# Kernel tuning notes

Hardware: AMD Instinct MI355X
Metric: run time of the kernel (lower is better)

The kernel has to match this reference:

```python
import jax, jax.numpy as jnp
import numpy as np

N = 50000   # nodes
E = 600000  # edges
D = 128     # in_channels
H = 32      # MLP hidden


def setup_inputs() -> dict:
    key = jax.random.key(0)
    ks = jax.random.split(key, 10)
    x = jax.random.normal(ks[0], (N, D), dtype=jnp.float32)
    edge_index = jax.random.randint(ks[1], (2, E), 0, N, dtype=jnp.int32)
    W_gcn = jax.random.normal(ks[2], (D, D), dtype=jnp.float32) / np.sqrt(D)
    b_gcn = jnp.zeros((D,), dtype=jnp.float32)
    w1 = jax.random.normal(ks[3], (D, H), dtype=jnp.float32) / np.sqrt(D)
    b1 = jnp.zeros((H,), dtype=jnp.float32)
    w2 = jax.random.normal(ks[4], (H, H), dtype=jnp.float32) / np.sqrt(H)
    b2 = jnp.zeros((H,), dtype=jnp.float32)
    w3 = jax.random.normal(ks[5], (H, 1), dtype=jnp.float32) / np.sqrt(H)
    b3 = jnp.zeros((1,), dtype=jnp.float32)
    return {"x": x, "edge_index": edge_index, "W_gcn": W_gcn, "b_gcn": b_gcn,
            "w1": w1, "b1": b1, "w2": w2, "b2": b2, "w3": w3, "b3": b3}


def _gcn_conv(x, edge_index, W, b):
    """PyG GCNConv: add self-loops, symmetric D^-1/2 (A+I) D^-1/2 normalization."""
    xw = x @ W  # [N, D]
    loop = jnp.arange(N, dtype=edge_index.dtype)
    row = jnp.concatenate([edge_index[0], loop])  # source
    col = jnp.concatenate([edge_index[1], loop])  # target
    deg = jax.ops.segment_sum(jnp.ones_like(col, dtype=xw.dtype), col, num_segments=N)
    dinv = jnp.where(deg > 0, jax.lax.rsqrt(deg), 0.0)
    norm = dinv[row] * dinv[col]              # [E+N]
    msg = xw[row] * norm[:, None]             # gather + scale, [E+N, D]
    out = jax.ops.segment_sum(msg, col, num_segments=N)  # scatter-add, [N, D]
    return out + b


def reference(x, edge_index, W_gcn, b_gcn, w1, b1, w2, b2, w3, b3):
    out = jax.nn.relu(_gcn_conv(x, edge_index, W_gcn, b_gcn))
    h = out + x                               # residual
    h = jax.nn.relu(h @ w1 + b1)
    h = jax.nn.relu(h @ w2 + b2)
    return h @ w3 + b3                        # [N, 1]
```

## Files before the change

kernel.cpp:

```cpp
#include <hip/hip_runtime.h>

#define DIM 128
#define HID 32
#define CAP 64
#define NFILL 512

typedef __attribute__((ext_vector_type(8))) short v8s;
typedef __attribute__((ext_vector_type(8))) unsigned short v8u;
typedef __attribute__((ext_vector_type(4))) float v4f;
typedef __attribute__((ext_vector_type(4))) int v4i;

static __device__ __forceinline__ unsigned short f2bf(float f) {
    unsigned int u = __float_as_uint(f);
    u += 0x7fffu + ((u >> 16) & 1u);
    return (unsigned short)(u >> 16);
}

__global__ __launch_bounds__(256) void prep_kernel(int2* __restrict__ csn,
                                                   const float* __restrict__ W,
                                                   unsigned short* __restrict__ wbt,
                                                   int n) {
    int gtid = (int)blockIdx.x * 256 + threadIdx.x;
    int nthr = (int)gridDim.x * 256;
    for (int i = gtid * 2; i < n; i += nthr * 2) {
        if (i + 1 < n) {
            *(int4*)&csn[i] = make_int4(0, 0, 0, 0);
        } else {
            csn[i] = make_int2(0, 0);
        }
    }
    for (int f = gtid; f < DIM * DIM; f += nthr) {
        int k = f >> 7, nn = f & 127;
        wbt[nn * 128 + k] = f2bf(W[f]);
    }
}

__global__ __launch_bounds__(256, 8) void gemm_fill_kernel(const float* __restrict__ x,
                                                           const unsigned short* __restrict__ wbt,
                                                           signed char* __restrict__ xwq,
                                                           int2* __restrict__ csn,
                                                           const int* __restrict__ ei,
                                                           int* __restrict__ srcs,
                                                           int n, int E) {
    int t = threadIdx.x;
    int b = (int)blockIdx.x;
    if (b < NFILL) {
        const int* col = ei + E;
        int* cnt = (int*)csn;
        const int xcd = b & 7;
        const int s = b >> 3;
        const int nslice = NFILL >> 3;
        const int octs = (E + 7) >> 3;
        const int ops = (octs + nslice - 1) / nslice;
        const int o0 = s * ops;
        const int o1 = min(o0 + ops, octs);
        for (int oi = o0 + t; oi < o1; oi += 256) {
            int base = oi * 8;
            if (base + 7 < E) {
                v4i ra = __builtin_nontemporal_load((const v4i*)&ei[base]);
                v4i rb = __builtin_nontemporal_load((const v4i*)&ei[base + 4]);
                v4i ca = __builtin_nontemporal_load((const v4i*)&col[base]);
                v4i cb = __builtin_nontemporal_load((const v4i*)&col[base + 4]);
#pragma unroll
                for (int u = 0; u < 4; ++u) {
                    int cc = ca[u];
                    if ((cc & 7) == xcd) {
                        int p = atomicAdd(&cnt[cc * 2], 1);
                        if (p < CAP) srcs[(cc << 6) + p] = ra[u];
                    }
                }
#pragma unroll
                for (int u = 0; u < 4; ++u) {
                    int cc = cb[u];
                    if ((cc & 7) == xcd) {
                        int p = atomicAdd(&cnt[cc * 2], 1);
                        if (p < CAP) srcs[(cc << 6) + p] = rb[u];
                    }
                }
            } else {
                for (int e = base; e < E; ++e) {
                    int cc = col[e];
                    if ((cc & 7) == xcd) {
                        int p = atomicAdd(&cnt[cc * 2], 1);
                        if (p < CAP) srcs[(cc << 6) + p] = ei[e];
                    }
                }
            }
        }
    } else {
        int tile = b - NFILL;
        int row0 = tile * 64;
        int w = t >> 6;
        int l = t & 63;
        int q = l >> 4;
        int mn = l & 15;
        int row = row0 + w * 16 + mn;

        v8s afrag[4];
        const float* xr = x + (size_t)row * DIM + q * 8;
#pragma unroll
        for (int kt = 0; kt < 4; ++kt) {
            float4 qa = make_float4(0.f, 0.f, 0.f, 0.f), qb = qa;
            if (row < n) {
                const float4* s4 = (const float4*)(xr + kt * 32);
                qa = s4[0];
                qb = s4[1];
            }
            v8u pk;
            pk[0] = f2bf(qa.x); pk[1] = f2bf(qa.y); pk[2] = f2bf(qa.z); pk[3] = f2bf(qa.w);
            pk[4] = f2bf(qb.x); pk[5] = f2bf(qb.y); pk[6] = f2bf(qb.z); pk[7] = f2bf(qb.w);
            afrag[kt] = (v8s)pk;
        }

        v4f acc[8];
        const unsigned short* wr = wbt + mn * 128 + q * 8;
#pragma unroll
        for (int ct = 0; ct < 8; ++ct) {
            acc[ct] = (v4f){0.f, 0.f, 0.f, 0.f};
#pragma unroll
            for (int kt = 0; kt < 4; ++kt) {
                v8s bfrag = *(const v8s*)(wr + ct * (16 * 128) + kt * 32);
                acc[ct] = __builtin_amdgcn_mfma_f32_16x16x32_bf16(afrag[kt], bfrag, acc[ct], 0, 0, 0);
            }
        }

        float m[4];
#pragma unroll
        for (int i = 0; i < 4; ++i) {
            float mm = 0.f;
#pragma unroll
            for (int ct = 0; ct < 8; ++ct) mm = fmaxf(mm, fabsf(acc[ct][i]));
            m[i] = mm;
        }
#pragma unroll
        for (int off = 1; off < 16; off <<= 1) {
#pragma unroll
            for (int i = 0; i < 4; ++i) m[i] = fmaxf(m[i], __shfl_xor(m[i], off));
        }
        float inv[4];
#pragma unroll
        for (int i = 0; i < 4; ++i) {
            m[i] = fmaxf(m[i], 1e-20f);
            inv[i] = 127.0f / m[i];
        }
        if (mn == 0) {
#pragma unroll
            for (int i = 0; i < 4; ++i) {
                int rowg = row0 + w * 16 + q * 4 + i;
                if (rowg < n) csn[rowg].y = __float_as_int(m[i] * (1.0f / 127.0f));
            }
        }
#pragma unroll
        for (int ct = 0; ct < 8; ++ct) {
            int colg = ct * 16 + mn;
#pragma unroll
            for (int i = 0; i < 4; ++i) {
                int rowg = row0 + w * 16 + q * 4 + i;
                if (rowg < n)
                    xwq[(size_t)rowg * DIM + colg] =
                        (signed char)__float2int_rn(acc[ct][i] * inv[i]);
            }
        }
    }
}

__global__ __launch_bounds__(256) void gather_tail_kernel(
    const signed char* __restrict__ xwq, const float* __restrict__ x,
    const int2* __restrict__ csn, const int* __restrict__ srcs,
    const float* __restrict__ b_gcn,
    const float* __restrict__ w1, const float* __restrict__ b1,
    const float* __restrict__ w2, const float* __restrict__ b2,
    const float* __restrict__ w3, const float* __restrict__ b3,
    float* __restrict__ out, int n) {
    __shared__ float hs[8][132];
    __shared__ float t1s[8][40];
    __shared__ int2 swl[8][32];
    int t = threadIdx.x;
    int g = t >> 5, j = t & 31;
    int node = blockIdx.x * 8 + g;
    if (node >= n) return;

    int beg = node << 6;
    int sj0 = srcs[beg + j];
    int2 cd = csn[node];
    int aq = ((const int*)(xwq + (size_t)node * DIM))[j];
    float4 xv = ((const float4*)(x + (size_t)node * DIM))[j];
    float4 bg = ((const float4*)b_gcn)[j];

    int d = min(cd.x, CAP);
    float scn = __int_as_float(cd.y);
    float ax = 0.f, ay = 0.f, az = 0.f, aw = 0.f;

    {
        int sj = min(max(sj0, 0), n - 1);
        int2 cw = csn[sj];
        float wj = (j < d) ? rsqrtf((float)cw.x + 1.0f) * __int_as_float(cw.y) : 0.f;
        swl[g][j] = make_int2(sj, __float_as_int(wj));
        int m = min(32, d);
        for (int i = 0; i < m; i += 16) {
            int v[16]; float wgt[16];
#pragma unroll
            for (int u = 0; u < 16; ++u) {
                int2 sw = swl[g][i + u];
                wgt[u] = __int_as_float(sw.y);
                v[u] = ((const int*)(xwq + (size_t)sw.x * DIM))[j];
            }
#pragma unroll
            for (int u = 0; u < 16; ++u) {
                ax += wgt[u] * (float)((v[u] << 24) >> 24);
                ay += wgt[u] * (float)((v[u] << 16) >> 24);
                az += wgt[u] * (float)((v[u] <<  8) >> 24);
                aw += wgt[u] * (float)( v[u]        >> 24);
            }
        }
    }
    for (int c0 = 32; c0 < d; c0 += 32) {
        int sj = 0; float wj = 0.f;
        if (c0 + j < d) {
            sj = srcs[beg + c0 + j];
            int2 cw = csn[sj];
            wj = rsqrtf((float)cw.x + 1.0f) * __int_as_float(cw.y);
        }
        swl[g][j] = make_int2(sj, __float_as_int(wj));
        int m = min(32, d - c0);
        for (int i = 0; i < m; i += 16) {
            int v[16]; float wgt[16];
#pragma unroll
            for (int u = 0; u < 16; ++u) {
                int2 sw = swl[g][i + u];
                wgt[u] = __int_as_float(sw.y);
                v[u] = ((const int*)(xwq + (size_t)sw.x * DIM))[j];
            }
#pragma unroll
            for (int u = 0; u < 16; ++u) {
                ax += wgt[u] * (float)((v[u] << 24) >> 24);
                ay += wgt[u] * (float)((v[u] << 16) >> 24);
                az += wgt[u] * (float)((v[u] <<  8) >> 24);
                aw += wgt[u] * (float)( v[u]        >> 24);
            }
        }
    }

    float di = rsqrtf((float)d + 1.0f);
    float sself = di * di * scn;
    float* h = &hs[g][4 * j];
    h[0] = fmaxf(di * ax + sself * (float)((aq << 24) >> 24) + bg.x, 0.f) + xv.x;
    h[1] = fmaxf(di * ay + sself * (float)((aq << 16) >> 24) + bg.y, 0.f) + xv.y;
    h[2] = fmaxf(di * az + sself * (float)((aq <<  8) >> 24) + bg.z, 0.f) + xv.z;
    h[3] = fmaxf(di * aw + sself * (float)( aq        >> 24) + bg.w, 0.f) + xv.w;
    float acc = b1[j];
    for (int k = 0; k < DIM; k += 4) {
        float4 hv = *(const float4*)&hs[g][k];
        acc += hv.x * w1[(k + 0) * HID + j];
        acc += hv.y * w1[(k + 1) * HID + j];
        acc += hv.z * w1[(k + 2) * HID + j];
        acc += hv.w * w1[(k + 3) * HID + j];
    }
    t1s[g][j] = fmaxf(acc, 0.0f);
    acc = b2[j];
    for (int k = 0; k < HID; k += 4) {
        float4 tv = *(const float4*)&t1s[g][k];
        acc += tv.x * w2[(k + 0) * HID + j];
        acc += tv.y * w2[(k + 1) * HID + j];
        acc += tv.z * w2[(k + 2) * HID + j];
        acc += tv.w * w2[(k + 3) * HID + j];
    }
    float v = fmaxf(acc, 0.0f) * w3[j];
#pragma unroll
    for (int off = 16; off > 0; off >>= 1) v += __shfl_down(v, off, 32);
    if (j == 0) out[node] = v + b3[0];
}

extern "C" void kernel_launch(void* const* d_in, const int* in_sizes, int n_in,
                              void* d_out, int out_size, void* d_ws, size_t ws_size,
                              hipStream_t stream) {
    const float* x     = (const float*)d_in[0];
    const int*   ei    = (const int*)d_in[1];
    const float* W_gcn = (const float*)d_in[2];
    const float* b_gcn = (const float*)d_in[3];
    const float* w1    = (const float*)d_in[4];
    const float* b1    = (const float*)d_in[5];
    const float* w2    = (const float*)d_in[6];
    const float* b2    = (const float*)d_in[7];
    const float* w3    = (const float*)d_in[8];
    const float* b3    = (const float*)d_in[9];
    float* out = (float*)d_out;

    const int n = in_sizes[0] / DIM;
    const int E = in_sizes[1] / 2;

    char* ws = (char*)d_ws;
    signed char* xwq = (signed char*)ws;
    char* p = ws + (size_t)n * DIM;
    p = (char*)(((size_t)p + 15) & ~(size_t)15);
    int2* csn = (int2*)p;            p += (size_t)n * sizeof(int2);
    p = (char*)(((size_t)p + 255) & ~(size_t)255);
    int*  srcs = (int*)p;            p += (size_t)n * CAP * sizeof(int);
    unsigned short* wbt = (unsigned short*)p;

    const int ngemm = (n + 63) / 64;

    prep_kernel<<<64, 256, 0, stream>>>(csn, W_gcn, wbt, n);
    gemm_fill_kernel<<<NFILL + ngemm, 256, 0, stream>>>(x, wbt, xwq, csn, ei,
                                                        srcs, n, E);
    gather_tail_kernel<<<(n + 7) / 8, 256, 0, stream>>>(xwq, x, csn, srcs,
                                                        b_gcn, w1, b1, w2, b2,
                                                        w3, b3, out, n);
}
```

Baseline: 171.0 us.

## Process two nodes per warp in gather tail and raise fill block count

The gather/MLP tail kernel now handles two nodes per 32-lane group (16 nodes per block), interleaving their neighbor loads to expose more memory-level parallelism and sharing w1/w2 weight loads across both nodes. The edge-fill portion of the fused GEMM/fill kernel gets four times as many blocks. This raises register pressure and may reduce occupancy. Nodes with uneven degrees leave some lanes idle while the busier node finishes.

```diff
diff --git a/kernel.cpp b/kernel.cpp
--- a/kernel.cpp
+++ b/kernel.cpp
@@ -3,7 +3,7 @@
 #define DIM 128
 #define HID 32
 #define CAP 64
-#define NFILL 512
+#define NFILL 2048
 
 typedef __attribute__((ext_vector_type(8))) short v8s;
 typedef __attribute__((ext_vector_type(8))) unsigned short v8u;
@@ -172,31 +172,92 @@
     const float* __restrict__ w2, const float* __restrict__ b2,
     const float* __restrict__ w3, const float* __restrict__ b3,
     float* __restrict__ out, int n) {
-    __shared__ float hs[8][132];
-    __shared__ float t1s[8][40];
-    __shared__ int2 swl[8][32];
+    __shared__ float hs[16][132];
+    __shared__ float t1s[16][40];
+    __shared__ int2 swl[16][32];
     int t = threadIdx.x;
     int g = t >> 5, j = t & 31;
-    int node = blockIdx.x * 8 + g;
-    if (node >= n) return;
-
-    int beg = node << 6;
-    int sj0 = srcs[beg + j];
-    int2 cd = csn[node];
-    int aq = ((const int*)(xwq + (size_t)node * DIM))[j];
-    float4 xv = ((const float4*)(x + (size_t)node * DIM))[j];
+    int base = (int)blockIdx.x * 16;
+    int nodeA = base + g;
+    int nodeB = base + 8 + g;
+    bool okA = nodeA < n, okB = nodeB < n;
+    int nA = okA ? nodeA : 0;
+    int nB = okB ? nodeB : 0;
+
+    int sA = srcs[(nA << 6) + j];
+    int sB = srcs[(nB << 6) + j];
+    int2 cdA = csn[nA];
+    int2 cdB = csn[nB];
+    int aqA = ((const int*)(xwq + (size_t)nA * DIM))[j];
+    int aqB = ((const int*)(xwq + (size_t)nB * DIM))[j];
+    float4 xvA = ((const float4*)(x + (size_t)nA * DIM))[j];
+    float4 xvB = ((const float4*)(x + (size_t)nB * DIM))[j];
     float4 bg = ((const float4*)b_gcn)[j];
 
-    int d = min(cd.x, CAP);
-    float scn = __int_as_float(cd.y);
-    float ax = 0.f, ay = 0.f, az = 0.f, aw = 0.f;
-
-    {
-        int sj = min(max(sj0, 0), n - 1);
-        int2 cw = csn[sj];
-        float wj = (j < d) ? rsqrtf((float)cw.x + 1.0f) * __int_as_float(cw.y) : 0.f;
+    int dA = okA ? min(cdA.x, CAP) : 0;
+    int dB = okB ? min(cdB.x, CAP) : 0;
+
+    sA = min(max(sA, 0), n - 1);
+    sB = min(max(sB, 0), n - 1);
+    int2 cwA = csn[sA];
+    int2 cwB = csn[sB];
+    float wjA = (j < dA) ? rsqrtf((float)cwA.x + 1.0f) * __int_as_float(cwA.y) : 0.f;
+    float wjB = (j < dB) ? rsqrtf((float)cwB.x + 1.0f) * __int_as_float(cwB.y) : 0.f;
+    swl[g][j]     = make_int2(sA, __float_as_int(wjA));
+    swl[g + 8][j] = make_int2(sB, __float_as_int(wjB));
+
+    float axA = 0.f, ayA = 0.f, azA = 0.f, awA = 0.f;
+    float axB = 0.f, ayB = 0.f, azB = 0.f, awB = 0.f;
+
+    int mA = min(32, dA), mB = min(32, dB);
+    int mm = max(mA, mB);
+    for (int i = 0; i < mm; i += 16) {
+        int va[16], vb[16]; float wa[16], wb[16];
+        bool doA = i < mA, doB = i < mB;
+        if (doA) {
+#pragma unroll
+            for (int u = 0; u < 16; ++u) {
+                int2 sw = swl[g][i + u];
+                wa[u] = __int_as_float(sw.y);
+                va[u] = ((const int*)(xwq + (size_t)sw.x * DIM))[j];
+            }
+        }
+        if (doB) {
+#pragma unroll
+            for (int u = 0; u < 16; ++u) {
+                int2 sw = swl[g + 8][i + u];
+                wb[u] = __int_as_float(sw.y);
+                vb[u] = ((const int*)(xwq + (size_t)sw.x * DIM))[j];
+            }
+        }
+        if (doA) {
+#pragma unroll
+            for (int u = 0; u < 16; ++u) {
+                axA += wa[u] * (float)((va[u] << 24) >> 24);
+                ayA += wa[u] * (float)((va[u] << 16) >> 24);
+                azA += wa[u] * (float)((va[u] <<  8) >> 24);
+                awA += wa[u] * (float)( va[u]        >> 24);
+            }
+        }
+        if (doB) {
+#pragma unroll
+            for (int u = 0; u < 16; ++u) {
+                axB += wb[u] * (float)((vb[u] << 24) >> 24);
+                ayB += wb[u] * (float)((vb[u] << 16) >> 24);
+                azB += wb[u] * (float)((vb[u] <<  8) >> 24);
+                awB += wb[u] * (float)( vb[u]        >> 24);
+            }
+        }
+    }
+    for (int c0 = 32; c0 < dA; c0 += 32) {
+        int sj = 0; float wj = 0.f;
+        if (c0 + j < dA) {
+            sj = srcs[(nA << 6) + c0 + j];
+            int2 cw = csn[sj];
+            wj = rsqrtf((float)cw.x + 1.0f) * __int_as_float(cw.y);
+        }
         swl[g][j] = make_int2(sj, __float_as_int(wj));
-        int m = min(32, d);
+        int m = min(32, dA - c0);
         for (int i = 0; i < m; i += 16) {
             int v[16]; float wgt[16];
 #pragma unroll
@@ -207,68 +268,92 @@
             }
 #pragma unroll
             for (int u = 0; u < 16; ++u) {
-                ax += wgt[u] * (float)((v[u] << 24) >> 24);
-                ay += wgt[u] * (float)((v[u] << 16) >> 24);
-                az += wgt[u] * (float)((v[u] <<  8) >> 24);
-                aw += wgt[u] * (float)( v[u]        >> 24);
-            }
-        }
-    }
-    for (int c0 = 32; c0 < d; c0 += 32) {
+                axA += wgt[u] * (float)((v[u] << 24) >> 24);
+                ayA += wgt[u] * (float)((v[u] << 16) >> 24);
+                azA += wgt[u] * (float)((v[u] <<  8) >> 24);
+                awA += wgt[u] * (float)( v[u]        >> 24);
+            }
+        }
+    }
+    for (int c0 = 32; c0 < dB; c0 += 32) {
         int sj = 0; float wj = 0.f;
-        if (c0 + j < d) {
-            sj = srcs[beg + c0 + j];
+        if (c0 + j < dB) {
+            sj = srcs[(nB << 6) + c0 + j];
             int2 cw = csn[sj];
             wj = rsqrtf((float)cw.x + 1.0f) * __int_as_float(cw.y);
         }
-        swl[g][j] = make_int2(sj, __float_as_int(wj));
-        int m = min(32, d - c0);
+        swl[g + 8][j] = make_int2(sj, __float_as_int(wj));
+        int m = min(32, dB - c0);
         for (int i = 0; i < m; i += 16) {
             int v[16]; float wgt[16];
 #pragma unroll
             for (int u = 0; u < 16; ++u) {
-                int2 sw = swl[g][i + u];
+                int2 sw = swl[g + 8][i + u];
                 wgt[u] = __int_as_float(sw.y);
                 v[u] = ((const int*)(xwq + (size_t)sw.x * DIM))[j];
             }
 #pragma unroll
             for (int u = 0; u < 16; ++u) {
-                ax += wgt[u] * (float)((v[u] << 24) >> 24);
-                ay += wgt[u] * (float)((v[u] << 16) >> 24);
-                az += wgt[u] * (float)((v[u] <<  8) >> 24);
-                aw += wgt[u] * (float)( v[u]        >> 24);
-            }
-        }
-    }
-
-    float di = rsqrtf((float)d + 1.0f);
-    float sself = di * di * scn;
-    float* h = &hs[g][4 * j];
-    h[0] = fmaxf(di * ax + sself * (float)((aq << 24) >> 24) + bg.x, 0.f) + xv.x;
-    h[1] = fmaxf(di * ay + sself * (float)((aq << 16) >> 24) + bg.y, 0.f) + xv.y;
-    h[2] = fmaxf(di * az + sself * (float)((aq <<  8) >> 24) + bg.z, 0.f) + xv.z;
-    h[3] = fmaxf(di * aw + sself * (float)( aq        >> 24) + bg.w, 0.f) + xv.w;
-    float acc = b1[j];
+                axB += wgt[u] * (float)((v[u] << 24) >> 24);
+                ayB += wgt[u] * (float)((v[u] << 16) >> 24);
+                azB += wgt[u] * (float)((v[u] <<  8) >> 24);
+                awB += wgt[u] * (float)( v[u]        >> 24);
+            }
+        }
+    }
+
+    float diA = rsqrtf((float)dA + 1.0f);
+    float ssA = diA * diA * __int_as_float(cdA.y);
+    float* hA = &hs[g][4 * j];
+    hA[0] = fmaxf(diA * axA + ssA * (float)((aqA << 24) >> 24) + bg.x, 0.f) + xvA.x;
+    hA[1] = fmaxf(diA * ayA + ssA * (float)((aqA << 16) >> 24) + bg.y, 0.f) + xvA.y;
+    hA[2] = fmaxf(diA * azA + ssA * (float)((aqA <<  8) >> 24) + bg.z, 0.f) + xvA.z;
+    hA[3] = fmaxf(diA * awA + ssA * (float)( aqA        >> 24) + bg.w, 0.f) + xvA.w;
+    float diB = rsqrtf((float)dB + 1.0f);
+    float ssB = diB * diB * __int_as_float(cdB.y);
+    float* hB = &hs[g + 8][4 * j];
+    hB[0] = fmaxf(diB * axB + ssB * (float)((aqB << 24) >> 24) + bg.x, 0.f) + xvB.x;
+    hB[1] = fmaxf(diB * ayB + ssB * (float)((aqB << 16) >> 24) + bg.y, 0.f) + xvB.y;
+    hB[2] = fmaxf(diB * azB + ssB * (float)((aqB <<  8) >> 24) + bg.z, 0.f) + xvB.z;
+    hB[3] = fmaxf(diB * awB + ssB * (float)( aqB        >> 24) + bg.w, 0.f) + xvB.w;
+
+    float a1A = b1[j], a1B = a1A;
     for (int k = 0; k < DIM; k += 4) {
-        float4 hv = *(const float4*)&hs[g][k];
-        acc += hv.x * w1[(k + 0) * HID + j];
-        acc += hv.y * w1[(k + 1) * HID + j];
-        acc += hv.z * w1[(k + 2) * HID + j];
-        acc += hv.w * w1[(k + 3) * HID + j];
-    }
-    t1s[g][j] = fmaxf(acc, 0.0f);
-    acc = b2[j];
+        float4 hvA = *(const float4*)&hs[g][k];
+        float4 hvB = *(const float4*)&hs[g + 8][k];
+        float w10 = w1[(k + 0) * HID + j];
+        float w11 = w1[(k + 1) * HID + j];
+        float w12 = w1[(k + 2) * HID + j];
+        float w13 = w1[(k + 3) * HID + j];
+        a1A += hvA.x * w10 + hvA.y * w11 + hvA.z * w12 + hvA.w * w13;
+        a1B += hvB.x * w10 + hvB.y * w11 + hvB.z * w12 + hvB.w * w13;
+    }
+    t1s[g][j] = fmaxf(a1A, 0.0f);
+    t1s[g + 8][j] = fmaxf(a1B, 0.0f);
+    float a2A = b2[j], a2B = a2A;
     for (int k = 0; k < HID; k += 4) {
-        float4 tv = *(const float4*)&t1s[g][k];
-        acc += tv.x * w2[(k + 0) * HID + j];
-        acc += tv.y * w2[(k + 1) * HID + j];
-        acc += tv.z * w2[(k + 2) * HID + j];
-        acc += tv.w * w2[(k + 3) * HID + j];
-    }
-    float v = fmaxf(acc, 0.0f) * w3[j];
-#pragma unroll
-    for (int off = 16; off > 0; off >>= 1) v += __shfl_down(v, off, 32);
-    if (j == 0) out[node] = v + b3[0];
+        float4 tvA = *(const float4*)&t1s[g][k];
+        float4 tvB = *(const float4*)&t1s[g + 8][k];
+        float w20 = w2[(k + 0) * HID + j];
+        float w21 = w2[(k + 1) * HID + j];
+        float w22 = w2[(k + 2) * HID + j];
+        float w23 = w2[(k + 3) * HID + j];
+        a2A += tvA.x * w20 + tvA.y * w21 + tvA.z * w22 + tvA.w * w23;
+        a2B += tvB.x * w20 + tvB.y * w21 + tvB.z * w22 + tvB.w * w23;
+    }
+    float w3j = w3[j];
+    float vA = fmaxf(a2A, 0.0f) * w3j;
+    float vB = fmaxf(a2B, 0.0f) * w3j;
+#pragma unroll
+    for (int off = 16; off > 0; off >>= 1) {
+        vA += __shfl_down(vA, off, 32);
+        vB += __shfl_down(vB, off, 32);
+    }
+    if (j == 0) {
+        float bb = b3[0];
+        if (okA) out[nodeA] = vA + bb;
+        if (okB) out[nodeB] = vB + bb;
+    }
 }
 
 extern "C" void kernel_launch(void* const* d_in, const int* in_sizes, int n_in,
@@ -303,7 +388,7 @@
     prep_kernel<<<64, 256, 0, stream>>>(csn, W_gcn, wbt, n);
     gemm_fill_kernel<<<NFILL + ngemm, 256, 0, stream>>>(x, wbt, xwq, csn, ei,
                                                         srcs, n, E);
-    gather_tail_kernel<<<(n + 7) / 8, 256, 0, stream>>>(xwq, x, csn, srcs,
-                                                        b_gcn, w1, b1, w2, b2,
-                                                        w3, b3, out, n);
-}
+    gather_tail_kernel<<<(n + 15) / 16, 256, 0, stream>>>(xwq, x, csn, srcs,
+                                                          b_gcn, w1, b1, w2, b2,
+                                                          w3, b3, out, n);
+}
```

Measured after the change: 173.0 us. Within noise of the previous version (+1.2%).
